# Kernel optimization log

Measured on AMD Instinct MI355X. Metric: run time of the kernel, lower is better.

The kernel has to match this reference:

```python
import jax, jax.numpy as jnp
import numpy as np

SEQ, IN, H = 64, 100000, 50


def setup_inputs() -> dict:
    key = jax.random.key(0)
    k0, k1, k2, k3, k4 = jax.random.split(key, 5)
    x = jax.random.normal(k0, (SEQ, 1, IN), dtype=jnp.float32) * 0.02
    Wi = jax.random.normal(k1, (IN, 4 * H), dtype=jnp.float32) * 0.01
    bi = jax.random.normal(k2, (4 * H,), dtype=jnp.float32) * 0.01
    Wh = jax.random.normal(k3, (H, 4 * H), dtype=jnp.float32) * 0.1
    bh = jax.random.normal(k4, (4 * H,), dtype=jnp.float32) * 0.01
    return {"x": x, "Wi": Wi, "bi": bi, "Wh": Wh, "bh": bh}


def reference(x, Wi, bi, Wh, bh):
    # x: [seq, batch=1, input_size] -- each row is a flattened ParameterList.
    # Precompute the input projection for all steps at once (one big GEMM),
    # same math as per-step input_weights(input) since it has no recurrence.
    gates_in = jnp.einsum('sbi,ig->sbg', x, Wi) + bi + bh  # [seq, 1, 4H]

    def step(carry, g_in):
        hx, cx = carry
        gates = g_in + hx @ Wh  # [1, 4H]
        i, f, g, o = jnp.split(gates, 4, axis=1)
        i = jax.nn.sigmoid(i)
        f = jax.nn.sigmoid(f)
        g = jnp.tanh(g)
        o = jax.nn.sigmoid(o)
        cy = f * cx + i * g
        hy = o * jnp.tanh(cy)
        return (hy, cy), None

    h0 = jnp.zeros((1, H), dtype=x.dtype)
    c0 = jnp.zeros((1, H), dtype=x.dtype)
    (h_final, _), _ = jax.lax.scan(step, (h0, c0), gates_in)
    # torch.squeeze(out_hidden): (1, H) -> (H,)
    return jnp.squeeze(h_final)
```

## Files before the change

### kernel.cpp

```cpp
#include <hip/hip_runtime.h>
#include <hip/hip_bf16.h>


#define K_DIM 100000
#define NG 200
#define NS 64
#define TK 32
#define NBLK 512
#define KSTRIDE (NBLK * TK)
#define CELLS (NS * NG)
#define CELLS4 (CELLS / 4)

static __device__ __forceinline__ float rl(float v, int l) {
    return __int_as_float(__builtin_amdgcn_readlane(__float_as_int(v), l));
}

__global__ __launch_bounds__(512, 4) void k1_gemm_partial(
    const float* __restrict__ x, const float* __restrict__ Wi,
    float* __restrict__ partial)
{
    __shared__ float4 ws4[TK * 50 + 16];

    const int tid  = threadIdx.x;
    const int lane = tid & 63;
    const int wave = tid >> 6;
    const int s0   = wave * 8;

    const int xrow  = s0 + (lane >> 3);
    const int xkoff = (lane & 7) << 2;
    const float* xbase = x + (size_t)xrow * K_DIM + xkoff;

    float4 acc4[8];
#pragma unroll
    for (int j = 0; j < 8; ++j) acc4[j] = make_float4(0.f, 0.f, 0.f, 0.f);

    int kt = blockIdx.x * TK;
    const float4* wi4 = (const float4*)Wi;

    float4 w0, w1, w2, w3 = make_float4(0.f, 0.f, 0.f, 0.f), xc, xn;
    {
        const float4* wt = wi4 + (size_t)kt * 50;
        w0 = wt[tid];
        w1 = wt[tid + 512];
        w2 = wt[tid + 1024];
        if (tid < 64) w3 = wt[tid + 1536];
        xc = *(const float4*)(xbase + kt);
    }

    for (; kt < K_DIM; kt += KSTRIDE) {
        __syncthreads();
        ws4[tid]        = w0;
        ws4[tid + 512]  = w1;
        ws4[tid + 1024] = w2;
        if (tid < 64) ws4[tid + 1536] = w3;
        __syncthreads();

        int ktn = kt + KSTRIDE;
        if (ktn < K_DIM) {
            const float4* wt = wi4 + (size_t)ktn * 50;
            w0 = wt[tid];
            w1 = wt[tid + 512];
            w2 = wt[tid + 1024];
            if (tid < 64) w3 = wt[tid + 1536];
            xn = *(const float4*)(xbase + ktn);
        }

#pragma unroll
        for (int q = 0; q < 8; ++q) {
#pragma unroll
            for (int kk = 0; kk < 4; ++kk) {
                float4 wv = ws4[(q * 4 + kk) * 50 + lane];
                float xcomp = (kk == 0) ? xc.x : (kk == 1) ? xc.y
                            : (kk == 2) ? xc.z : xc.w;
#pragma unroll
                for (int r = 0; r < 8; ++r) {
                    float xv = rl(xcomp, r * 8 + q);
                    acc4[r].x = fmaf(wv.x, xv, acc4[r].x);
                    acc4[r].y = fmaf(wv.y, xv, acc4[r].y);
                    acc4[r].z = fmaf(wv.z, xv, acc4[r].z);
                    acc4[r].w = fmaf(wv.w, xv, acc4[r].w);
                }
            }
        }
        xc = xn;
    }

    if (lane < 50) {
        float4* pout = (float4*)(partial + (size_t)blockIdx.x * CELLS) + lane;
#pragma unroll
        for (int si = 0; si < 8; ++si)
            pout[(s0 + si) * 50] = acc4[si];
    }
}

__global__ __launch_bounds__(512) void k2_reduce(
    const float* __restrict__ partial, const float* __restrict__ bi,
    const float* __restrict__ bh, float* __restrict__ gates)
{
    __shared__ float4 red[512];
    const int tid   = threadIdx.x;
    const int fid   = tid & 15;
    const int slice = tid >> 4;
    const int g4    = blockIdx.x * 16 + fid;

    const float4* p4 = (const float4*)partial;
    float4 sum = make_float4(0.f, 0.f, 0.f, 0.f);
#pragma unroll 4
    for (int b = slice * 16; b < slice * 16 + 16; ++b) {
        float4 v = p4[(size_t)b * CELLS4 + g4];
        sum.x += v.x; sum.y += v.y; sum.z += v.z; sum.w += v.w;
    }
    red[tid] = sum;
    __syncthreads();
    if (tid < 16) {
        float4 tot = red[tid];
#pragma unroll
        for (int p = 1; p < 32; ++p) {
            float4 v = red[p * 16 + tid];
            tot.x += v.x; tot.y += v.y; tot.z += v.z; tot.w += v.w;
        }
        int gg = (g4 * 4) % NG;
        float4 b1 = *(const float4*)(bi + gg);
        float4 b2 = *(const float4*)(bh + gg);
        tot.x += b1.x + b2.x; tot.y += b1.y + b2.y;
        tot.z += b1.z + b2.z; tot.w += b1.w + b2.w;
        ((float4*)gates)[g4] = tot;
    }
}

__global__ __launch_bounds__(256) void k3_lstm(
    const float* __restrict__ gates, const float* __restrict__ Wh,
    float* __restrict__ out)
{
    __shared__ float gz[CELLS];
    __shared__ float h_lds[64];
    __shared__ float act_lds[NG];
    const int g = threadIdx.x;

    for (int i = g; i < CELLS; i += 256) gz[i] = gates[i];

    float wh[50];
    if (g < NG) {
#pragma unroll
        for (int j = 0; j < 50; ++j) wh[j] = Wh[j * NG + g];
    }
    if (g < 64) h_lds[g] = 0.f;
    float c = 0.f, h = 0.f;
    const bool is_cell_gate = (g >= 100 && g < 150);
    __syncthreads();

    for (int s = 0; s < 64; ++s) {
        if (g < NG) {
            float a0 = gz[s * NG + g], a1 = 0.f, a2 = 0.f, a3 = 0.f;
#pragma unroll
            for (int jj = 0; jj < 48; jj += 4) {
                float4 h4 = *(const float4*)(h_lds + jj);
                a0 = fmaf(h4.x, wh[jj],     a0);
                a1 = fmaf(h4.y, wh[jj + 1], a1);
                a2 = fmaf(h4.z, wh[jj + 2], a2);
                a3 = fmaf(h4.w, wh[jj + 3], a3);
            }
            {
                float2 h2 = *(const float2*)(h_lds + 48);
                a0 = fmaf(h2.x, wh[48], a0);
                a1 = fmaf(h2.y, wh[49], a1);
            }
            float z = (a0 + a1) + (a2 + a3);
            float e   = __expf(-z);
            float sig = 1.f / (1.f + e);
            float e2  = e * e;
            float th  = (1.f - e2) / (1.f + e2);
            act_lds[g] = is_cell_gate ? th : sig;
        }
        __syncthreads();
        if (g < 50) {
            float iv = act_lds[g];
            float fv = act_lds[50 + g];
            float gv = act_lds[100 + g];
            float ov = act_lds[150 + g];
            c = fmaf(fv, c, iv * gv);
            float e2c = __expf(-2.f * c);
            h = ov * (1.f - e2c) / (1.f + e2c);
            h_lds[g] = h;
        }
        __syncthreads();
    }
    if (g < 50) out[g] = h;
}

extern "C" void kernel_launch(void* const* d_in, const int* in_sizes, int n_in,
                              void* d_out, int out_size, void* d_ws, size_t ws_size,
                              hipStream_t stream)
{
    const float* x  = (const float*)d_in[0];
    const float* Wi = (const float*)d_in[1];
    const float* bi = (const float*)d_in[2];
    const float* Wh = (const float*)d_in[3];
    const float* bh = (const float*)d_in[4];
    float* out = (float*)d_out;

    float* partial = (float*)d_ws;
    float* gates   = partial + (size_t)NBLK * CELLS;

    k1_gemm_partial<<<NBLK, 512, 0, stream>>>(x, Wi, partial);
    k2_reduce<<<CELLS4 / 16, 512, 0, stream>>>(partial, bi, bh, gates);
    k3_lstm<<<1, 256, 0, stream>>>(gates, Wh, out);
}
```

Measured before the change: 207.8 us.

## Use split-bf16 MFMA for input projection GEMM instead of FP32 FMA

```diff
diff --git a/kernel.cpp b/kernel.cpp
--- a/kernel.cpp
+++ b/kernel.cpp
@@ -7,89 +7,154 @@
 #define NS 64
 #define TK 32
 #define NBLK 512
-#define KSTRIDE (NBLK * TK)
+#define NTILES 3125
 #define CELLS (NS * NG)
 #define CELLS4 (CELLS / 4)
-
-static __device__ __forceinline__ float rl(float v, int l) {
-    return __int_as_float(__builtin_amdgcn_readlane(__float_as_int(v), l));
-}
-
-__global__ __launch_bounds__(512, 4) void k1_gemm_partial(
+#define ROWU 40
+
+typedef unsigned short u16;
+typedef unsigned int   u32;
+typedef __bf16 bf16x8 __attribute__((ext_vector_type(8)));
+typedef float  f32x16 __attribute__((ext_vector_type(16)));
+
+static __device__ __forceinline__ u32 rne16(float f) {
+    u32 u = __float_as_uint(f);
+    return (u + 0x7FFFu + ((u >> 16) & 1u)) >> 16;
+}
+static __device__ __forceinline__ void split_hl(float f, u32& h, u32& l) {
+    u32 u  = __float_as_uint(f);
+    u32 hb = u & 0xFFFF0000u;
+    h = hb >> 16;
+    l = rne16(f - __uint_as_float(hb));
+}
+static __device__ __forceinline__ void split4(float4 v, u32 h[4], u32 l[4]) {
+    split_hl(v.x, h[0], l[0]); split_hl(v.y, h[1], l[1]);
+    split_hl(v.z, h[2], l[2]); split_hl(v.w, h[3], l[3]);
+}
+static __device__ __forceinline__ f32x16 mfma_bf(uint4 a, uint4 b, f32x16 c) {
+    return __builtin_amdgcn_mfma_f32_32x32x16_bf16(
+        __builtin_bit_cast(bf16x8, a), __builtin_bit_cast(bf16x8, b), c, 0, 0, 0);
+}
+
+__global__ __launch_bounds__(256, 2) void k1_gemm_partial(
     const float* __restrict__ x, const float* __restrict__ Wi,
     float* __restrict__ partial)
 {
-    __shared__ float4 ws4[TK * 50 + 16];
-
-    const int tid  = threadIdx.x;
-    const int lane = tid & 63;
-    const int wave = tid >> 6;
-    const int s0   = wave * 8;
-
-    const int xrow  = s0 + (lane >> 3);
-    const int xkoff = (lane & 7) << 2;
-    const float* xbase = x + (size_t)xrow * K_DIM + xkoff;
-
-    float4 acc4[8];
-#pragma unroll
-    for (int j = 0; j < 8; ++j) acc4[j] = make_float4(0.f, 0.f, 0.f, 0.f);
-
-    int kt = blockIdx.x * TK;
-    const float4* wi4 = (const float4*)Wi;
-
-    float4 w0, w1, w2, w3 = make_float4(0.f, 0.f, 0.f, 0.f), xc, xn;
+    __shared__ __align__(16) u16 WH[224 * ROWU];
+    __shared__ __align__(16) u16 WL[224 * ROWU];
+    __shared__ __align__(16) u16 XH[64 * ROWU];
+    __shared__ __align__(16) u16 XL[64 * ROWU];
+
+    const int t    = threadIdx.x;
+    const int lane = t & 63;
+    const int wave = t >> 6;
+    const int m    = lane & 31;
+    const int h    = lane >> 5;
+    const int stile = wave >> 1;
+    const int gset  = wave & 1;
+
     {
-        const float4* wt = wi4 + (size_t)kt * 50;
-        w0 = wt[tid];
-        w1 = wt[tid + 512];
-        w2 = wt[tid + 1024];
-        if (tid < 64) w3 = wt[tid + 1536];
-        xc = *(const float4*)(xbase + kt);
-    }
-
-    for (; kt < K_DIM; kt += KSTRIDE) {
-        __syncthreads();
-        ws4[tid]        = w0;
-        ws4[tid + 512]  = w1;
-        ws4[tid + 1024] = w2;
-        if (tid < 64) ws4[tid + 1536] = w3;
-        __syncthreads();
-
-        int ktn = kt + KSTRIDE;
-        if (ktn < K_DIM) {
-            const float4* wt = wi4 + (size_t)ktn * 50;
-            w0 = wt[tid];
-            w1 = wt[tid + 512];
-            w2 = wt[tid + 1024];
-            if (tid < 64) w3 = wt[tid + 1536];
-            xn = *(const float4*)(xbase + ktn);
-        }
-
-#pragma unroll
-        for (int q = 0; q < 8; ++q) {
-#pragma unroll
-            for (int kk = 0; kk < 4; ++kk) {
-                float4 wv = ws4[(q * 4 + kk) * 50 + lane];
-                float xcomp = (kk == 0) ? xc.x : (kk == 1) ? xc.y
-                            : (kk == 2) ? xc.z : xc.w;
-#pragma unroll
-                for (int r = 0; r < 8; ++r) {
-                    float xv = rl(xcomp, r * 8 + q);
-                    acc4[r].x = fmaf(wv.x, xv, acc4[r].x);
-                    acc4[r].y = fmaf(wv.y, xv, acc4[r].y);
-                    acc4[r].z = fmaf(wv.z, xv, acc4[r].z);
-                    acc4[r].w = fmaf(wv.w, xv, acc4[r].w);
-                }
-            }
-        }
-        xc = xn;
-    }
-
-    if (lane < 50) {
-        float4* pout = (float4*)(partial + (size_t)blockIdx.x * CELLS) + lane;
-#pragma unroll
-        for (int si = 0; si < 8; ++si)
-            pout[(s0 + si) * 50] = acc4[si];
+        u32* zh = (u32*)&WH[200 * ROWU];
+        u32* zl = (u32*)&WL[200 * ROWU];
+        for (int i = t; i < 24 * ROWU / 2; i += 256) { zh[i] = 0; zl[i] = 0; }
+    }
+
+    const int a_g4 = (t & 7) + 8 * ((t >> 6) & 3);
+    const int a_k4 = (t >> 3) & 7;
+    int b_g4 = -1, b_k4 = 0;
+    if (t < 128)      { int tau = t + 256; b_g4 = (tau & 7) + 8 * (tau >> 6); b_k4 = (tau >> 3) & 7; }
+    else if (t >= 240){ int idx = t - 240; b_g4 = 48 + (idx & 1); b_k4 = idx >> 1; }
+    const int xs0 = t >> 3, xk0 = t & 7;
+    const int xs1 = (t + 256) >> 3, xk1 = t & 7;
+
+    float4 wa[4], wb[4], xa, xb;
+    auto do_loads = [&](int ti) {
+        const size_t kt = (size_t)ti * TK;
+#pragma unroll
+        for (int j = 0; j < 4; ++j)
+            wa[j] = *(const float4*)(Wi + (kt + a_k4 * 4 + j) * NG + a_g4 * 4);
+        if (b_g4 >= 0) {
+#pragma unroll
+            for (int j = 0; j < 4; ++j)
+                wb[j] = *(const float4*)(Wi + (kt + b_k4 * 4 + j) * NG + b_g4 * 4);
+        }
+        xa = *(const float4*)(x + (size_t)xs0 * K_DIM + kt + xk0 * 4);
+        xb = *(const float4*)(x + (size_t)xs1 * K_DIM + kt + xk1 * 4);
+    };
+    auto stage_wi = [&](const float4 r[4], int g4, int k4) {
+        u32 hw[4][4], lw[4][4];
+#pragma unroll
+        for (int j = 0; j < 4; ++j) split4(r[j], hw[j], lw[j]);
+#pragma unroll
+        for (int j2 = 0; j2 < 4; ++j2) {
+            int off = (4 * g4 + j2) * ROWU + k4 * 4;
+            *(uint2*)&WH[off] = make_uint2(hw[0][j2] | (hw[1][j2] << 16),
+                                           hw[2][j2] | (hw[3][j2] << 16));
+            *(uint2*)&WL[off] = make_uint2(lw[0][j2] | (lw[1][j2] << 16),
+                                           lw[2][j2] | (lw[3][j2] << 16));
+        }
+    };
+    auto stage_x = [&](float4 v, int s, int k4) {
+        u32 hh[4], ll[4];
+        split4(v, hh, ll);
+        int off = s * ROWU + k4 * 4;
+        *(uint2*)&XH[off] = make_uint2(hh[0] | (hh[1] << 16), hh[2] | (hh[3] << 16));
+        *(uint2*)&XL[off] = make_uint2(ll[0] | (ll[1] << 16), ll[2] | (ll[3] << 16));
+    };
+
+    f32x16 acc[4];
+#pragma unroll
+    for (int tt = 0; tt < 4; ++tt)
+#pragma unroll
+        for (int r = 0; r < 16; ++r) acc[tt][r] = 0.f;
+
+    const int aoff = (stile * 32 + m) * ROWU + h * 8;
+    int boff[4];
+#pragma unroll
+    for (int tt = 0; tt < 4; ++tt) {
+        int gt = gset ? (4 + (tt == 3 ? 2 : tt)) : tt;
+        boff[tt] = (gt * 32 + m) * ROWU + h * 8;
+    }
+
+    do_loads(blockIdx.x);
+    for (int ti = blockIdx.x; ti < NTILES; ti += NBLK) {
+        __syncthreads();
+        stage_wi(wa, a_g4, a_k4);
+        if (b_g4 >= 0) stage_wi(wb, b_g4, b_k4);
+        stage_x(xa, xs0, xk0);
+        stage_x(xb, xs1, xk1);
+        __syncthreads();
+
+        int tin = ti + NBLK;
+        if (tin < NTILES) do_loads(tin);
+
+#pragma unroll
+        for (int kk = 0; kk < 2; ++kk) {
+            uint4 ah = *(const uint4*)&XH[aoff + kk * 16];
+            uint4 al = *(const uint4*)&XL[aoff + kk * 16];
+#pragma unroll
+            for (int tt = 0; tt < 4; ++tt) {
+                uint4 bh = *(const uint4*)&WH[boff[tt] + kk * 16];
+                uint4 bl = *(const uint4*)&WL[boff[tt] + kk * 16];
+                acc[tt] = mfma_bf(ah, bh, acc[tt]);
+                acc[tt] = mfma_bf(ah, bl, acc[tt]);
+                acc[tt] = mfma_bf(al, bh, acc[tt]);
+            }
+        }
+    }
+
+    float* base = partial + (size_t)blockIdx.x * CELLS;
+#pragma unroll
+    for (int tt = 0; tt < 4; ++tt) {
+        if (gset && tt == 3) continue;
+        int g = (gset ? 4 + tt : tt) * 32 + m;
+        if (g < NG) {
+#pragma unroll
+            for (int r = 0; r < 16; ++r) {
+                int srow = stile * 32 + (r & 3) + 8 * (r >> 2) + 4 * h;
+                base[srow * NG + g] = acc[tt][r];
+            }
+        }
     }
 }
 
@@ -202,7 +267,7 @@
     float* partial = (float*)d_ws;
     float* gates   = partial + (size_t)NBLK * CELLS;
 
-    k1_gemm_partial<<<NBLK, 512, 0, stream>>>(x, Wi, partial);
+    k1_gemm_partial<<<NBLK, 256, 0, stream>>>(x, Wi, partial);
     k2_reduce<<<CELLS4 / 16, 512, 0, stream>>>(partial, bi, bh, gates);
     k3_lstm<<<1, 256, 0, stream>>>(gates, Wh, out);
 }
```

After: 188.6 us. -9.3%, faster.
